# Kernel tuning notes

Measured on AMD Instinct MI355X. Metric: run time of the kernel, lower is better.

The kernel has to match this reference:

```python
import jax, jax.numpy as jnp
import numpy as np
from jax import lax

B, C_IN, H, W = 32, 96, 48, 48
D = C_IN          # d_inner = expand(1) * in_features
K, N, DT_RANK = 2, 16, 6   # k_group, d_state, ceil(D/16)


def setup_inputs() -> dict:
    key = jax.random.key(0)
    ks = jax.random.split(key, 10)
    s = 0.02
    return {
        "x": jax.random.normal(ks[0], (B, C_IN, H, W), jnp.float32),
        "in_proj_w": jax.random.normal(ks[1], (D, C_IN)) * s,
        "in_proj_b": jnp.zeros((D,)),
        "skip_w": jax.random.normal(ks[2], (1, 1, 5)) * s,
        "skip_b": jnp.zeros((1,)),
        "conv2d_w": jax.random.normal(ks[3], (D, 1, 3, 3)) * s,
        "conv2d_b": jnp.zeros((D,)),
        "local_w": jax.random.normal(ks[4], (D, 1, 3, 3)) * s,
        "local_b": jnp.zeros((D,)),
        "bn_gamma": jnp.ones((D,)),
        "bn_beta": jnp.zeros((D,)),
        "x_proj_w": jax.random.normal(ks[5], (K, DT_RANK + 2 * N, D)) * s,
        "dt_projs_w": jax.random.normal(ks[6], (K, D, DT_RANK)) * s,
        "dt_projs_b": jax.random.normal(ks[7], (K, D)) * s,
        "A_logs": jnp.tile(jnp.log(jnp.arange(1, N + 1, dtype=jnp.float32))[None], (K * D, 1)),
        "Ds": jnp.ones((K * D,)),
        "norm_gamma": jnp.ones((D,)),
        "norm_beta": jnp.zeros((D,)),
        "out_proj_w": jax.random.normal(ks[8], (C_IN, D)) * s,
        "out_proj_b": jnp.zeros((C_IN,)),
    }


def _dwconv2d(x, w, bias):
    # depthwise 3x3, NCHW
    y = lax.conv_general_dilated(x, w, (1, 1), "SAME", feature_group_count=x.shape[1],
                                 dimension_numbers=("NCHW", "OIHW", "NCHW"))
    return y + bias[None, :, None, None]


def _forward(x, in_proj_w, in_proj_b, skip_w, skip_b, conv2d_w, conv2d_b,
             local_w, local_b, bn_gamma, bn_beta, x_proj_w, dt_projs_w,
             dt_projs_b, A_logs, Ds, norm_gamma, norm_beta, out_proj_w, out_proj_b):
    b, c, h, w = x.shape
    L = h * w
    x_in = jnp.transpose(x, (0, 2, 3, 1))                       # [B,H,W,C]
    # skip gate: Conv1d(1,1,k=5) over channel axis of the spatial mean
    zm = jnp.mean(x_in, axis=(1, 2))[:, None, :]                # [B,1,C]
    z = lax.conv_general_dilated(zm, skip_w, (1,), "SAME",
                                 dimension_numbers=("NCH", "OIH", "NCH")) + skip_b[None, :, None]
    z = z[:, None]                                              # [B,1,1,C]
    x_feat = jnp.transpose(x_in @ in_proj_w.T + in_proj_b, (0, 3, 1, 2))  # [B,D,H,W]
    x_conv = jax.nn.silu(_dwconv2d(x_feat, conv2d_w, conv2d_b))
    # ---- dynamic center-similarity ordering (computed under no_grad) ----
    xc = lax.stop_gradient(x_conv)
    xf = xc.reshape(b, D, L)
    xn = xf / jnp.maximum(jnp.linalg.norm(xf, axis=1, keepdims=True), 1e-12)
    cf = xc[:, :, h // 2, w // 2]                               # [B,D]
    cn = cf / jnp.maximum(jnp.linalg.norm(cf, axis=1, keepdims=True), 1e-12)
    sim = jnp.einsum("bdl,bd->bl", xn, cn)
    sort_idx = jnp.argsort(-sim, axis=1)                        # descending similarity
    inv_idx = jnp.argsort(sort_idx, axis=1)
    # ---- DynamicCenterScan: sorted sequence and its reverse (k_group=2) ----
    xseq = jnp.take_along_axis(x_conv.reshape(b, D, L), sort_idx[:, None, :], axis=2)
    xs = jnp.stack([xseq, jnp.flip(xseq, -1)], axis=1)          # [B,K,D,L]
    # ---- SS2D selective-scan core ----
    x_dbl = jnp.einsum("bkdl,kcd->bkcl", xs, x_proj_w)
    dts, Bs, Cs = jnp.split(x_dbl, [DT_RANK, DT_RANK + N], axis=2)
    dts = jnp.einsum("bkrl,kdr->bkdl", dts, dt_projs_w)
    dts = jax.nn.softplus(dts + dt_projs_b[None, :, :, None])   # [B,K,D,L]
    A = -jnp.exp(A_logs.reshape(K, D, N))                       # [K,D,N]

    def step(hst, t):
        dt_l, B_l, C_l, x_l = t                                 # [B,K,D],[B,K,N],[B,K,N],[B,K,D]
        dA = jnp.exp(dt_l[..., None] * A)                       # [B,K,D,N]
        hst = dA * hst + (dt_l * x_l)[..., None] * B_l[:, :, None, :]
        y = jnp.einsum("bkdn,bkn->bkd", hst, C_l)
        return hst, y

    tmove = lambda a: jnp.moveaxis(a, -1, 0)
    h0 = jnp.zeros((b, K, D, N), x.dtype)
    _, ys_t = lax.scan(step, h0, (tmove(dts), tmove(Bs), tmove(Cs), tmove(xs)))
    ys = jnp.moveaxis(ys_t, 0, -1) + Ds.reshape(K, D)[None, :, :, None] * xs  # [B,K,D,L]
    # ---- DynamicCenterMerge: un-flip, sum directions, inverse permutation ----
    y = ys[:, 0] + jnp.flip(ys[:, 1], -1)
    y = jnp.take_along_axis(y, inv_idx[:, None, :], axis=2).reshape(b, D, h, w)
    # out_norm: LayerNorm over channels
    yl = jnp.transpose(y, (0, 2, 3, 1))
    mu = jnp.mean(yl, -1, keepdims=True)
    var = jnp.var(yl, -1, keepdims=True)
    yl = (yl - mu) / jnp.sqrt(var + 1e-5) * norm_gamma + norm_beta
    out_mamba = jnp.transpose(yl, (0, 3, 1, 2))
    # local path: depthwise conv + BatchNorm (batch stats, train mode) + SiLU
    lc = _dwconv2d(x_conv, local_w, local_b)
    bm = jnp.mean(lc, (0, 2, 3))
    bv = jnp.var(lc, (0, 2, 3))
    lc = (lc - bm[None, :, None, None]) * (bn_gamma / jnp.sqrt(bv + 1e-5))[None, :, None, None] + bn_beta[None, :, None, None]
    lc = jax.nn.silu(lc)
    out = out_mamba + lc
    # softmax over dim=1 of z (singleton) == all-ones gate; kept for faithfulness
    out = jnp.transpose(out, (0, 2, 3, 1)) * jax.nn.softmax(z, axis=1)
    out = out @ out_proj_w.T + out_proj_b
    return jnp.transpose(out, (0, 3, 1, 2))


def reference(x, in_proj_w, in_proj_b, skip_w, skip_b, conv2d_w, conv2d_b,
              local_w, local_b, bn_gamma, bn_beta, x_proj_w, dt_projs_w,
              dt_projs_b, A_logs, Ds, norm_gamma, norm_beta, out_proj_w, out_proj_b):
    return _forward(x, in_proj_w, in_proj_b, skip_w, skip_b, conv2d_w, conv2d_b,
                    local_w, local_b, bn_gamma, bn_beta, x_proj_w, dt_projs_w,
                    dt_projs_b, A_logs, Ds, norm_gamma, norm_beta, out_proj_w, out_proj_b)
```

## Files before the change

### kernel.cpp

```cpp
#include <hip/hip_runtime.h>
#include <hip/hip_bf16.h>


typedef __hip_bfloat16 bf16;
typedef float v2f __attribute__((ext_vector_type(2)));
typedef float v4f __attribute__((ext_vector_type(4)));
#define SH2(V, a, b) __builtin_shufflevector(V, V, a, b)

__device__ __forceinline__ float b2f(bf16 v) { return __bfloat162float(v); }
__device__ __forceinline__ float ldu(const void* p, int i, bool f32) {
  if (f32) return ((const float*)p)[i];
  return b2f(((const bf16*)p)[i]);
}
__device__ __forceinline__ float rcp_f(float x) { return __builtin_amdgcn_rcpf(x); }

#define LL 2304
#define NSEG 72

#define W_INT  0
#define B_IN   9216
#define W_C2D  9312
#define B_C2D  10176
#define W_LOC  10272
#define B_LOC  11136
#define BN_G   11232
#define BN_B   11328
#define W_XPT  11424
#define W_DT   19104
#define B_DT   20256
#define A2OF   20448
#define DSOF   23520
#define LN_G   23712
#define LN_B   23808
#define W_OUTT 23904
#define B_OUT  33120
#define WBUF_N 33280ul

#define O_WBUF  0ul
#define O_XFEAT 33280ul
#define O_XCONV 7111168ul
#define O_SIM   14189056ul
#define O_SIDX  14262784ul
#define O_XST   14336512ul
#define O_XSTD  21414400ul
#define O_RBUF  28492288ul
#define O_BC    29671936ul
#define O_DSUM  34390528ul
#define O_YMLM  34832896ul
#define O_STATS 41910784ul
#define O_AFLG  41910976ul
#define O_SCSH  41911040ul
#define O_FLAG  41911232ul
#define O_END   41911296ul

__global__ void k_detect(const void* x, float* flag) {
  int i = threadIdx.x;
  bool bad = false;
  const bf16* xb = (const bf16*)x;
#pragma unroll
  for (int r = 0; r < 4; ++r) {
    float v = b2f(xb[r * 64 + i]);
    if (!(fabsf(v) <= 1e4f)) bad = true;
  }
  bool any = __any(bad);
  if (i == 0) flag[0] = any ? 1.f : 0.f;
}

__global__ void k_prep(const void* ipw, const void* ipb, const void* c2w, const void* c2b,
                       const void* lw, const void* lb, const void* bng, const void* bnb,
                       const void* xpw, const void* dtw, const void* dtb, const void* alog,
                       const void* dss, const void* ng, const void* nb, const void* opw,
                       const void* opb, float* wb, const float* flag, float* aflag) {
  bool f = flag[0] > 0.5f;
  int i = blockIdx.x * 256 + threadIdx.x;
  if (i < 9216) {
    int r = i / 96, c = i % 96;
    wb[W_INT + c * 96 + r] = ldu(ipw, i, f);
    wb[W_OUTT + c * 96 + r] = ldu(opw, i, f);
  }
  if (i < 96) {
    wb[B_IN + i] = ldu(ipb, i, f); wb[B_C2D + i] = ldu(c2b, i, f); wb[B_LOC + i] = ldu(lb, i, f);
    wb[BN_G + i] = ldu(bng, i, f); wb[BN_B + i] = ldu(bnb, i, f); wb[LN_G + i] = ldu(ng, i, f);
    wb[LN_B + i] = ldu(nb, i, f); wb[B_OUT + i] = ldu(opb, i, f);
  }
  if (i < 864) { wb[W_C2D + i] = ldu(c2w, i, f); wb[W_LOC + i] = ldu(lw, i, f); }
  if (i < 7296) {
    int k = i / 3648, c = (i / 96) % 38, d = i % 96;
    wb[W_XPT + d * 80 + k * 38 + c] = ldu(xpw, i, f);
  }
  if (i < 1152) wb[W_DT + i] = ldu(dtw, i, f);
  if (i < 192) { wb[B_DT + i] = ldu(dtb, i, f); wb[DSOF + i] = ldu(dss, i, f); }
  if (i < 3072) {
    float av = expf(ldu(alog, i, f));
    wb[A2OF + i] = -av * 1.4426950408889634f;
    int n = i % 16;
    if (fabsf(av - (float)(n + 1)) > 1e-3f * (n + 1)) atomicAdd(aflag, 1.f);
  }
}

__global__ __launch_bounds__(128, 4)
void k_inproj(const void* __restrict__ x, const float* __restrict__ wb,
              float* __restrict__ xfeat, const float* __restrict__ flag) {
  int b = blockIdx.x / 72;
  int rest = blockIdx.x % 72;
  int q = rest / 18;
  int l = (rest % 18) * 128 + threadIdx.x;
  float acc[24];
#pragma unroll
  for (int j = 0; j < 24; ++j) acc[j] = wb[B_IN + q * 24 + j];
  bool f = flag[0] > 0.5f;
  if (f) {
    const float* xf = (const float*)x;
#pragma unroll 2
    for (int c = 0; c < 96; ++c) {
      float xc = xf[(b * 96 + c) * LL + l];
      const float* wr = wb + W_INT + c * 96 + q * 24;
#pragma unroll
      for (int j = 0; j < 24; ++j) acc[j] += xc * wr[j];
    }
  } else {
    const bf16* xb = (const bf16*)x;
#pragma unroll 2
    for (int c = 0; c < 96; ++c) {
      float xc = b2f(xb[(b * 96 + c) * LL + l]);
      const float* wr = wb + W_INT + c * 96 + q * 24;
#pragma unroll
      for (int j = 0; j < 24; ++j) acc[j] += xc * wr[j];
    }
  }
#pragma unroll
  for (int j = 0; j < 24; ++j) xfeat[(b * 96 + q * 24 + j) * LL + l] = acc[j];
}

__global__ __launch_bounds__(256, 8)
void k_conv_silu(const float* __restrict__ xfeat, const float* __restrict__ wb,
                 float* __restrict__ xconv) {
  int t = blockIdx.x * 256 + threadIdx.x;
  int l = t % LL; int d = (t / LL) % 96; int b = t / (LL * 96);
  int h = l / 48, w = l % 48;
  const float* wr = wb + W_C2D + d * 9;
  const float* src = xfeat + (b * 96 + d) * LL;
  float acc = wb[B_C2D + d];
#pragma unroll
  for (int ki = 0; ki < 3; ++ki) {
    int hh = h + ki - 1; if (hh < 0 || hh >= 48) continue;
#pragma unroll
    for (int kj = 0; kj < 3; ++kj) {
      int ww = w + kj - 1; if (ww < 0 || ww >= 48) continue;
      acc += src[hh * 48 + ww] * wr[ki * 3 + kj];
    }
  }
  xconv[t] = acc / (1.f + expf(-acc));
}

__global__ __launch_bounds__(256, 8)
void k_sim(const float* __restrict__ xconv, float* __restrict__ sim) {
  int b = blockIdx.x / 9;
  int l = (blockIdx.x % 9) * 256 + threadIdx.x;
  const float* base = xconv + (size_t)b * 96 * LL;
  float dot = 0, nrm = 0, cn = 0;
  for (int d = 0; d < 96; ++d) {
    float v = base[d * LL + l];
    float c = base[d * LL + 1176];
    dot += v * c; nrm += v * v; cn += c * c;
  }
  float den = fmaxf(sqrtf(nrm), 1e-12f) * fmaxf(sqrtf(cn), 1e-12f);
  sim[b * LL + l] = dot / den;
}

__global__ __launch_bounds__(256, 8)
void k_rank(const float* __restrict__ sim, int* __restrict__ sidx) {
  __shared__ unsigned su[LL];
  int b = blockIdx.x / 36;
  int part = blockIdx.x % 36;
  const float* sp = sim + b * LL;
  for (int i = threadIdx.x; i < LL; i += 256) {
    unsigned u = __float_as_uint(sp[i]);
    u = (u >> 31) ? ~u : (u | 0x80000000u);
    su[i] = u;
  }
  __syncthreads();
  int lq = threadIdx.x >> 2;
  int ch = threadIdx.x & 3;
  int l = part * 64 + lq;
  unsigned ui = su[l];
  int rank = 0;
  const uint4* s4 = (const uint4*)su;
#pragma unroll 4
  for (int it = 0; it < 144; ++it) {
    int m = 4 * it + ch;
    uint4 U = s4[m];
    int j = 4 * m;
    rank += (int)(U.x > ui) + (int)((U.x == ui) & (j + 0 < l));
    rank += (int)(U.y > ui) + (int)((U.y == ui) & (j + 1 < l));
    rank += (int)(U.z > ui) + (int)((U.z == ui) & (j + 2 < l));
    rank += (int)(U.w > ui) + (int)((U.w == ui) & (j + 3 < l));
  }
  rank += __shfl_xor(rank, 1);
  rank += __shfl_xor(rank, 2);
  if (ch == 0) sidx[b * LL + rank] = l;
}

__global__ __launch_bounds__(256, 8)
void k_gatherd(const float* __restrict__ xconv, const int* __restrict__ sidx,
               float* __restrict__ xstd) {
  int t = blockIdx.x * 256 + threadIdx.x;
  int l = t % LL; int d = (t / LL) % 96; int b = t / (LL * 96);
  int p = sidx[b * LL + l];
  xstd[t] = xconv[((size_t)b * 96 + d) * LL + p];
}

__global__ __launch_bounds__(256, 4)
void k_tr_dl(const float* __restrict__ in, float* __restrict__ out) {
  __shared__ float tile[64 * 97];
  int b = blockIdx.x / 36;
  int l0 = (blockIdx.x % 36) * 64;
#pragma unroll
  for (int it = 0; it < 24; ++it) {
    int idx = it * 256 + threadIdx.x;
    int d = idx / 64, j = idx % 64;
    tile[j * 97 + d] = in[((size_t)b * 96 + d) * LL + l0 + j];
  }
  __syncthreads();
#pragma unroll
  for (int it = 0; it < 24; ++it) {
    int idx = it * 256 + threadIdx.x;
    int r = idx / 96, c = idx % 96;
    out[((size_t)b * LL + l0 + r) * 96 + c] = tile[r * 97 + c];
  }
}

__global__ __launch_bounds__(256, 4)
void k_tr_ld(const float* __restrict__ in, float* __restrict__ out) {
  __shared__ float tile[64 * 97];
  int b = blockIdx.x / 36;
  int l0 = (blockIdx.x % 36) * 64;
#pragma unroll
  for (int it = 0; it < 24; ++it) {
    int idx = it * 256 + threadIdx.x;
    int r = idx / 96, c = idx % 96;
    tile[r * 97 + c] = in[((size_t)b * LL + l0 + r) * 96 + c];
  }
  __syncthreads();
#pragma unroll
  for (int it = 0; it < 24; ++it) {
    int idx = it * 256 + threadIdx.x;
    int d = idx / 64, j = idx % 64;
    out[((size_t)b * 96 + d) * LL + l0 + j] = tile[j * 97 + d];
  }
}

__global__ __launch_bounds__(128, 4)
void k_xdbl(const float* __restrict__ xstd, const float* __restrict__ wb,
            float* __restrict__ rbuf, float* __restrict__ bc) {
  int kq = blockIdx.x / 576;
  int r = blockIdx.x % 576;
  int b = r / 18;
  int l = (r % 18) * 128 + threadIdx.x;
  float acc[38];
#pragma unroll
  for (int j = 0; j < 38; ++j) acc[j] = 0.f;
#pragma unroll 2
  for (int c = 0; c < 96; ++c) {
    float xc = xstd[((size_t)b * 96 + c) * LL + l];
    const float* wr = wb + W_XPT + c * 80 + kq * 38;
#pragma unroll
    for (int j = 0; j < 38; ++j) acc[j] += xc * wr[j];
  }
  int lout = kq ? (LL - 1 - l) : l;
  float4* r4 = (float4*)(rbuf + ((size_t)(b * 2 + kq) * LL + lout) * 8);
  r4[0] = make_float4(acc[0], acc[1], acc[2], acc[3]);
  r4[1] = make_float4(acc[4], acc[5], 0.f, 0.f);
  float4* b4 = (float4*)(bc + ((size_t)(b * 2 + kq) * LL + lout) * 32);
#pragma unroll
  for (int i = 0; i < 8; ++i)
    b4[i] = make_float4(acc[6 + 4 * i], acc[7 + 4 * i], acc[8 + 4 * i], acc[9 + 4 * i]);
}

__global__ __launch_bounds__(192, 3)
void k_scan1(const float* __restrict__ rbuf, const float* __restrict__ bc,
             const float* __restrict__ xst, const float* __restrict__ wb,
             float* __restrict__ dsum, float* __restrict__ hend,
             const float* __restrict__ aflag) {
  __shared__ float sbc[2][1024];
  __shared__ float srr[2][256];
  int sub = threadIdx.x / 96;
  int tid = threadIdx.x - sub * 96;
  int unit = blockIdx.x * 2 + sub;
  int s = unit % 72; int k = (unit / 72) % 2; int b = unit / 144;
  int lbase = (b * 2 + k) * LL + s * 32;
  long long lk0 = k ? (LL - 1 - s * 32) : (s * 32);
  long long stp = k ? -96 : 96;
  const float* xp = xst + (size_t)b * LL * 96 + lk0 * 96 + tid;
  float xv[32];
#pragma unroll
  for (int t = 0; t < 32; ++t) xv[t] = xp[t * stp];
  {
    const float4* bsrc = (const float4*)(bc + (size_t)lbase * 32);
    float4* bdst = (float4*)sbc[sub];
    for (int i = tid; i < 256; i += 96) bdst[i] = bsrc[i];
    const float4* rsrc = (const float4*)(rbuf + (size_t)lbase * 8);
    float4* rdst = (float4*)srr[sub];
    if (tid < 64) rdst[tid] = rsrc[tid];
  }
  __syncthreads();
  int d = tid;
  float wd[6];
#pragma unroll
  for (int j = 0; j < 6; ++j) wd[j] = wb[W_DT + (k * 96 + d) * 6 + j];
  float bd = wb[B_DT + k * 96 + d];
  float ds = 0.f;
  v2f h2[8];
#pragma unroll
  for (int j = 0; j < 8; ++j) h2[j] = (v2f){0.f, 0.f};
  bool fast = (aflag[0] == 0.f);
  if (fast) {
    const v4f* bq4 = (const v4f*)sbc[sub];
    const v4f* rq4 = (const v4f*)srr[sub];
#pragma unroll
    for (int t = 0; t < 32; ++t) {
      v4f r0 = rq4[t * 2], r1 = rq4[t * 2 + 1];
      float a = bd + r0.x * wd[0] + r0.y * wd[1] + r0.z * wd[2]
                   + r0.w * wd[3] + r1.x * wd[4] + r1.y * wd[5];
      float ea = __expf(a);
      float p1 = rcp_f(1.f + ea);
      float dtv = (a > 20.f) ? a : -0.69314718055994531f * __log2f(p1);
      ds += dtv;
      float dtx = dtv * xv[t];
      v2f dt2 = {dtx, dtx};
      float p2s = p1 * p1;
      v2f P1 = {p1, p2s};
      v2f P2 = P1 * (v2f){p2s, p2s};
      float p4s = P2.y;
      v2f P3 = P1 * (v2f){p4s, p4s};
      v2f P4 = P2 * (v2f){p4s, p4s};
      float p8s = P4.y;
      v2f P5 = P1 * (v2f){p8s, p8s};
      v2f P6 = P2 * (v2f){p8s, p8s};
      v2f P7 = P3 * (v2f){p8s, p8s};
      v2f P8 = P4 * (v2f){p8s, p8s};
      v4f B0 = bq4[t * 8 + 0], B1 = bq4[t * 8 + 1];
      v4f B2 = bq4[t * 8 + 2], B3 = bq4[t * 8 + 3];
      h2[0] = P1 * h2[0] + dt2 * SH2(B0, 0, 1);
      h2[1] = P2 * h2[1] + dt2 * SH2(B0, 2, 3);
      h2[2] = P3 * h2[2] + dt2 * SH2(B1, 0, 1);
      h2[3] = P4 * h2[3] + dt2 * SH2(B1, 2, 3);
      h2[4] = P5 * h2[4] + dt2 * SH2(B2, 0, 1);
      h2[5] = P6 * h2[5] + dt2 * SH2(B2, 2, 3);
      h2[6] = P7 * h2[6] + dt2 * SH2(B3, 0, 1);
      h2[7] = P8 * h2[7] + dt2 * SH2(B3, 2, 3);
    }
  } else {
    float a2[16], hh[16];
#pragma unroll
    for (int n = 0; n < 16; ++n) { a2[n] = wb[A2OF + (k * 96 + d) * 16 + n]; hh[n] = 0.f; }
#pragma unroll 4
    for (int t = 0; t < 32; ++t) {
      const float* rr = &srr[sub][t * 8];
      float a = bd + rr[0] * wd[0] + rr[1] * wd[1] + rr[2] * wd[2]
                   + rr[3] * wd[3] + rr[4] * wd[4] + rr[5] * wd[5];
      float dtv = (a > 20.f) ? a : log1pf(expf(a));
      ds += dtv;
      float dtx = dtv * xv[t];
      const float* bcl = &sbc[sub][t * 32];
#pragma unroll
      for (int n = 0; n < 16; ++n) hh[n] = exp2f(dtv * a2[n]) * hh[n] + dtx * bcl[n];
    }
#pragma unroll
    for (int j = 0; j < 8; ++j) h2[j] = (v2f){hh[2 * j], hh[2 * j + 1]};
  }
  dsum[((b * 2 + k) * 96 + d) * NSEG + s] = ds;
  float4* ho = (float4*)(hend + (((size_t)(b * 2 + k) * NSEG + s) * 96 + d) * 16);
  ho[0] = make_float4(h2[0].x, h2[0].y, h2[1].x, h2[1].y);
  ho[1] = make_float4(h2[2].x, h2[2].y, h2[3].x, h2[3].y);
  ho[2] = make_float4(h2[4].x, h2[4].y, h2[5].x, h2[5].y);
  ho[3] = make_float4(h2[6].x, h2[6].y, h2[7].x, h2[7].y);
}

__global__ __launch_bounds__(256, 4)
void k_scan2(const float* __restrict__ dsum, const float* __restrict__ hend,
             const float* __restrict__ wb, float* __restrict__ hstart) {
  int t = blockIdx.x * 256 + threadIdx.x;
  int n = t % 16; int d = (t / 16) % 96; int k = (t / 1536) % 2; int b = t / 3072;
  float a2 = wb[A2OF + (k * 96 + d) * 16 + n];
  float h = 0.f;
  int rowd = ((b * 2 + k) * 96 + d) * NSEG;
#pragma unroll 8
  for (int s = 0; s < NSEG; ++s) {
    size_t idx = (((size_t)(b * 2 + k) * NSEG + s) * 96 + d) * 16 + n;
    hstart[idx] = h;
    h = exp2f(a2 * dsum[rowd + s]) * h + hend[idx];
  }
}

__global__ __launch_bounds__(192, 3)
void k_scan3ln(const float* __restrict__ rbuf, const float* __restrict__ bc,
               const float* __restrict__ xst, const float* __restrict__ wb,
               const float* __restrict__ hstart, const int* __restrict__ sidx,
               float* __restrict__ ymlm, const float* __restrict__ aflag) {
  __shared__ float yA[32 * 97];
  __shared__ float yB[32 * 97];
  __shared__ float sbc[2][1024];
  __shared__ float srr[2][256];
  __shared__ float smu[32], srs[32];
  int b = blockIdx.x / NSEG;
  int u = blockIdx.x % NSEG;
  int t = threadIdx.x;
  int sub = t / 96;
  int d = t - sub * 96;
  int k = sub;
  int seg = sub ? (NSEG - 1 - u) : u;
  int lbase = (b * 2 + k) * LL + seg * 32;
  long long lk0 = k ? (LL - 1 - seg * 32) : (seg * 32);
  long long stp = k ? -96 : 96;
  const float* xp = xst + (size_t)b * LL * 96 + lk0 * 96 + d;
  float xv[32];
#pragma unroll
  for (int i = 0; i < 32; ++i) xv[i] = xp[i * stp];
  {
    const float4* bsrc = (const float4*)(bc + (size_t)lbase * 32);
    float4* bdst = (float4*)sbc[sub];
    for (int i = d; i < 256; i += 96) bdst[i] = bsrc[i];
    const float4* rsrc = (const float4*)(rbuf + (size_t)lbase * 8);
    float4* rdst = (float4*)srr[sub];
    if (d < 64) rdst[d] = rsrc[d];
  }
  __syncthreads();
  {
    float* yacc = sub ? yB : yA;
    float wd[6];
#pragma unroll
    for (int j = 0; j < 6; ++j) wd[j] = wb[W_DT + (k * 96 + d) * 6 + j];
    float bd = wb[B_DT + k * 96 + d];
    float Dv = wb[DSOF + k * 96 + d];
    const float* hi = hstart + (((size_t)(b * 2 + k) * NSEG + seg) * 96 + d) * 16;
    bool fast = (aflag[0] == 0.f);
    if (fast) {
      const v4f* hi4 = (const v4f*)hi;
      v4f H0 = hi4[0], H1 = hi4[1], H2 = hi4[2], H3 = hi4[3];
      v2f h2[8];
      h2[0] = SH2(H0, 0, 1); h2[1] = SH2(H0, 2, 3);
      h2[2] = SH2(H1, 0, 1); h2[3] = SH2(H1, 2, 3);
      h2[4] = SH2(H2, 0, 1); h2[5] = SH2(H2, 2, 3);
      h2[6] = SH2(H3, 0, 1); h2[7] = SH2(H3, 2, 3);
      const v4f* bq4 = (const v4f*)sbc[sub];
      const v4f* rq4 = (const v4f*)srr[sub];
#pragma unroll
      for (int i = 0; i < 32; ++i) {
        v4f r0 = rq4[i * 2], r1 = rq4[i * 2 + 1];
        float a = bd + r0.x * wd[0] + r0.y * wd[1] + r0.z * wd[2]
                     + r0.w * wd[3] + r1.x * wd[4] + r1.y * wd[5];
        float ea = __expf(a);
        float p1 = rcp_f(1.f + ea);
        float dtv = (a > 20.f) ? a : -0.69314718055994531f * __log2f(p1);
        float dtx = dtv * xv[i];
        v2f dt2 = {dtx, dtx};
        float p2s = p1 * p1;
        v2f P1 = {p1, p2s};
        v2f P2 = P1 * (v2f){p2s, p2s};
        float p4s = P2.y;
        v2f P3 = P1 * (v2f){p4s, p4s};
        v2f P4 = P2 * (v2f){p4s, p4s};
        float p8s = P4.y;
        v2f P5 = P1 * (v2f){p8s, p8s};
        v2f P6 = P2 * (v2f){p8s, p8s};
        v2f P7 = P3 * (v2f){p8s, p8s};
        v2f P8 = P4 * (v2f){p8s, p8s};
        v4f B0 = bq4[i * 8 + 0], B1 = bq4[i * 8 + 1];
        v4f B2 = bq4[i * 8 + 2], B3 = bq4[i * 8 + 3];
        v4f C0 = bq4[i * 8 + 4], C1 = bq4[i * 8 + 5];
        v4f C2 = bq4[i * 8 + 6], C3 = bq4[i * 8 + 7];
        v2f y2;
        h2[0] = P1 * h2[0] + dt2 * SH2(B0, 0, 1); y2  = h2[0] * SH2(C0, 0, 1);
        h2[1] = P2 * h2[1] + dt2 * SH2(B0, 2, 3); y2 += h2[1] * SH2(C0, 2, 3);
        h2[2] = P3 * h2[2] + dt2 * SH2(B1, 0, 1); y2 += h2[2] * SH2(C1, 0, 1);
        h2[3] = P4 * h2[3] + dt2 * SH2(B1, 2, 3); y2 += h2[3] * SH2(C1, 2, 3);
        h2[4] = P5 * h2[4] + dt2 * SH2(B2, 0, 1); y2 += h2[4] * SH2(C2, 0, 1);
        h2[5] = P6 * h2[5] + dt2 * SH2(B2, 2, 3); y2 += h2[5] * SH2(C2, 2, 3);
        h2[6] = P7 * h2[6] + dt2 * SH2(B3, 0, 1); y2 += h2[6] * SH2(C3, 0, 1);
        h2[7] = P8 * h2[7] + dt2 * SH2(B3, 2, 3); y2 += h2[7] * SH2(C3, 2, 3);
        int qloc = k ? (31 - i) : i;
        yacc[qloc * 97 + d] = y2.x + y2.y + Dv * xv[i];
      }
    } else {
      float a2[16], hh[16];
#pragma unroll
      for (int n = 0; n < 16; ++n) { a2[n] = wb[A2OF + (k * 96 + d) * 16 + n]; hh[n] = hi[n]; }
#pragma unroll 4
      for (int i = 0; i < 32; ++i) {
        const float* rr = &srr[sub][i * 8];
        float a = bd + rr[0] * wd[0] + rr[1] * wd[1] + rr[2] * wd[2]
                     + rr[3] * wd[3] + rr[4] * wd[4] + rr[5] * wd[5];
        float dtv = (a > 20.f) ? a : log1pf(expf(a));
        float dtx = dtv * xv[i];
        const float* bcl = &sbc[sub][i * 32];
        float y = 0.f;
#pragma unroll
        for (int n = 0; n < 16; ++n) {
          hh[n] = exp2f(dtv * a2[n]) * hh[n] + dtx * bcl[n];
          y += hh[n] * bcl[16 + n];
        }
        int qloc = k ? (31 - i) : i;
        yacc[qloc * 97 + d] = y + Dv * xv[i];
      }
    }
  }
  __syncthreads();
  if (t < 32) {
    float sum = 0, ss = 0;
#pragma unroll
    for (int dd = 0; dd < 96; ++dd) {
      float v = yA[t * 97 + dd] + yB[t * 97 + dd];
      sum += v; ss += v * v;
    }
    float mu = sum * (1.f / 96.f);
    float var = ss * (1.f / 96.f) - mu * mu;
    smu[t] = mu;
    srs[t] = rsqrtf(var + 1e-5f);
  }
  __syncthreads();
  {
    int r = t / 6, c0 = (t % 6) * 16;
    int q = u * 32 + r;
    int p = sidx[b * LL + q];
    float mu = smu[r], rs = srs[r];
    float tmp[16];
#pragma unroll
    for (int j = 0; j < 16; ++j) {
      int dd = c0 + j;
      tmp[j] = (yA[r * 97 + dd] + yB[r * 97 + dd] - mu) * rs * wb[LN_G + dd] + wb[LN_B + dd];
    }
    float4* o4 = (float4*)(ymlm + ((size_t)b * LL + p) * 96 + c0);
    o4[0] = make_float4(tmp[0], tmp[1], tmp[2], tmp[3]);
    o4[1] = make_float4(tmp[4], tmp[5], tmp[6], tmp[7]);
    o4[2] = make_float4(tmp[8], tmp[9], tmp[10], tmp[11]);
    o4[3] = make_float4(tmp[12], tmp[13], tmp[14], tmp[15]);
  }
}

__global__ __launch_bounds__(256, 8)
void k_convlc_bn(const float* __restrict__ xconv, const float* __restrict__ wb,
                 float* __restrict__ lcbuf, float* __restrict__ stats) {
  int bd = blockIdx.x;
  int b = bd / 96, d = bd % 96;
  const float* src = xconv + (size_t)(b * 96 + d) * LL;
  const float* wr = wb + W_LOC + d * 9;
  float bias = wb[B_LOC + d];
  float s1 = 0, s2 = 0;
  for (int l = threadIdx.x; l < LL; l += 256) {
    int h = l / 48, w = l % 48;
    float acc = bias;
#pragma unroll
    for (int ki = 0; ki < 3; ++ki) {
      int hh = h + ki - 1; if (hh < 0 || hh >= 48) continue;
#pragma unroll
      for (int kj = 0; kj < 3; ++kj) {
        int ww = w + kj - 1; if (ww < 0 || ww >= 48) continue;
        acc += src[hh * 48 + ww] * wr[ki * 3 + kj];
      }
    }
    lcbuf[(size_t)(b * 96 + d) * LL + l] = acc;
    s1 += acc; s2 += acc * acc;
  }
  __shared__ float r1[256], r2[256];
  r1[threadIdx.x] = s1; r2[threadIdx.x] = s2; __syncthreads();
  for (int o = 128; o > 0; o >>= 1) {
    if (threadIdx.x < o) { r1[threadIdx.x] += r1[threadIdx.x + o]; r2[threadIdx.x] += r2[threadIdx.x + o]; }
    __syncthreads();
  }
  if (threadIdx.x == 0) { atomicAdd(&stats[d], r1[0]); atomicAdd(&stats[96 + d], r2[0]); }
}

__global__ void k_bnfin(const float* __restrict__ stats, const float* __restrict__ wb,
                        float* __restrict__ scsh) {
  int d = threadIdx.x; if (d >= 96) return;
  float mean = stats[d] * (1.f / 73728.f);
  float var = stats[96 + d] * (1.f / 73728.f) - mean * mean;
  float sc = wb[BN_G + d] * rsqrtf(var + 1e-5f);
  scsh[d] = sc; scsh[96 + d] = wb[BN_B + d] - mean * sc;
}

__global__ __launch_bounds__(128, 4)
void k_final(const float* __restrict__ lcbuf, const float* __restrict__ ymdm,
             const float* __restrict__ wb, const float* __restrict__ scsh,
             void* __restrict__ out, const float* __restrict__ flag) {
  int b = blockIdx.x / 72;
  int rest = blockIdx.x % 72;
  int q = rest / 18;
  int l = (rest % 18) * 128 + threadIdx.x;
  float acc[24];
#pragma unroll
  for (int j = 0; j < 24; ++j) acc[j] = wb[B_OUT + q * 24 + j];
#pragma unroll 2
  for (int d = 0; d < 96; ++d) {
    float lc = lcbuf[((size_t)b * 96 + d) * LL + l] * scsh[d] + scsh[96 + d];
    float vd = lc * rcp_f(1.f + __expf(-lc)) + ymdm[((size_t)b * 96 + d) * LL + l];
    const float* wr = wb + W_OUTT + d * 96 + q * 24;
#pragma unroll
    for (int j = 0; j < 24; ++j) acc[j] += vd * wr[j];
  }
  bool f = flag[0] > 0.5f;
  if (f) {
    float* of = (float*)out;
#pragma unroll
    for (int j = 0; j < 24; ++j) of[(b * 96 + q * 24 + j) * LL + l] = acc[j];
  } else {
    bf16* ob = (bf16*)out;
#pragma unroll
    for (int j = 0; j < 24; ++j) ob[(b * 96 + q * 24 + j) * LL + l] = __float2bfloat16(acc[j]);
  }
}

extern "C" void kernel_launch(void* const* d_in, const int* in_sizes, int n_in,
                              void* d_out, int out_size, void* d_ws, size_t ws_size,
                              hipStream_t stream) {
  if (ws_size < O_END * sizeof(float)) return;
  float* ws = (float*)d_ws;
  float* wb    = ws + O_WBUF;
  float* xfeat = ws + O_XFEAT;
  float* xconv = ws + O_XCONV;
  float* sim   = ws + O_SIM;
  int*   sidx  = (int*)(ws + O_SIDX);
  float* xst   = ws + O_XST;
  float* xstd  = ws + O_XSTD;
  float* rbuf  = ws + O_RBUF;
  float* bc    = ws + O_BC;
  float* dsum  = ws + O_DSUM;
  float* ymlm  = ws + O_YMLM;
  float* stats = ws + O_STATS;
  float* aflag = ws + O_AFLG;
  float* scsh  = ws + O_SCSH;
  float* flag  = ws + O_FLAG;
  float* hend   = xfeat;
  float* hstart = xstd;
  float* ymdm   = xfeat;
  float* lcbuf  = xst;

  hipMemsetAsync(stats, 0, 256 * sizeof(float), stream);
  k_detect<<<1, 64, 0, stream>>>(d_in[0], flag);
  k_prep<<<36, 256, 0, stream>>>(
      d_in[1], d_in[2], d_in[5], d_in[6], d_in[7], d_in[8], d_in[9], d_in[10],
      d_in[11], d_in[12], d_in[13], d_in[14], d_in[15], d_in[16], d_in[17], d_in[18],
      d_in[19], wb, flag, aflag);
  k_inproj<<<2304, 128, 0, stream>>>(d_in[0], wb, xfeat, flag);
  k_conv_silu<<<27648, 256, 0, stream>>>(xfeat, wb, xconv);
  k_sim<<<288, 256, 0, stream>>>(xconv, sim);
  k_rank<<<1152, 256, 0, stream>>>(sim, sidx);
  k_gatherd<<<27648, 256, 0, stream>>>(xconv, sidx, xstd);
  k_tr_dl<<<1152, 256, 0, stream>>>(xstd, xst);
  k_xdbl<<<1152, 128, 0, stream>>>(xstd, wb, rbuf, bc);
  k_scan1<<<2304, 192, 0, stream>>>(rbuf, bc, xst, wb, dsum, hend, aflag);
  k_scan2<<<384, 256, 0, stream>>>(dsum, hend, wb, hstart);
  k_scan3ln<<<2304, 192, 0, stream>>>(rbuf, bc, xst, wb, hstart, sidx, ymlm, aflag);
  k_tr_ld<<<1152, 256, 0, stream>>>(ymlm, ymdm);
  k_convlc_bn<<<3072, 256, 0, stream>>>(xconv, wb, lcbuf, stats);
  k_bnfin<<<1, 96, 0, stream>>>(stats, wb, scsh);
  k_final<<<2304, 128, 0, stream>>>(lcbuf, ymdm, wb, scsh, d_out, flag);
}
```

Baseline: 500.8 us.

## Fuse gather with transpose, drop output transpose, parallelize LayerNorm stats

Merges the per-element gather and the D-to-L transpose into one kernel that gathers a tile into shared memory and writes both layouts. It also removes the final L-to-D transpose by having k_final read the L-major buffer directly, and spreads the LayerNorm row reduction across all 192 threads instead of 32. Together these cut two kernel launches and several full-tensor round trips through global memory. The cost is that k_final now reads 96 floats per thread at a stride of 96 floats across lanes, which is an uncoalesced access pattern.

```diff
diff --git a/kernel.cpp b/kernel.cpp
--- a/kernel.cpp
+++ b/kernel.cpp
@@ -201,52 +201,34 @@
   if (ch == 0) sidx[b * LL + rank] = l;
 }
 
-__global__ __launch_bounds__(256, 8)
-void k_gatherd(const float* __restrict__ xconv, const int* __restrict__ sidx,
-               float* __restrict__ xstd) {
-  int t = blockIdx.x * 256 + threadIdx.x;
-  int l = t % LL; int d = (t / LL) % 96; int b = t / (LL * 96);
-  int p = sidx[b * LL + l];
-  xstd[t] = xconv[((size_t)b * 96 + d) * LL + p];
-}
-
 __global__ __launch_bounds__(256, 4)
-void k_tr_dl(const float* __restrict__ in, float* __restrict__ out) {
+void k_gather2(const float* __restrict__ xconv, const int* __restrict__ sidx,
+               float* __restrict__ xstd, float* __restrict__ xst) {
   __shared__ float tile[64 * 97];
+  __shared__ int sp[64];
   int b = blockIdx.x / 36;
   int l0 = (blockIdx.x % 36) * 64;
+  if (threadIdx.x < 64) sp[threadIdx.x] = sidx[b * LL + l0 + threadIdx.x];
+  __syncthreads();
+  const float* base = xconv + (size_t)b * 96 * LL;
 #pragma unroll
   for (int it = 0; it < 24; ++it) {
     int idx = it * 256 + threadIdx.x;
     int d = idx / 64, j = idx % 64;
-    tile[j * 97 + d] = in[((size_t)b * 96 + d) * LL + l0 + j];
+    tile[j * 97 + d] = base[d * LL + sp[j]];
   }
   __syncthreads();
 #pragma unroll
   for (int it = 0; it < 24; ++it) {
     int idx = it * 256 + threadIdx.x;
     int r = idx / 96, c = idx % 96;
-    out[((size_t)b * LL + l0 + r) * 96 + c] = tile[r * 97 + c];
-  }
-}
-
-__global__ __launch_bounds__(256, 4)
-void k_tr_ld(const float* __restrict__ in, float* __restrict__ out) {
-  __shared__ float tile[64 * 97];
-  int b = blockIdx.x / 36;
-  int l0 = (blockIdx.x % 36) * 64;
-#pragma unroll
-  for (int it = 0; it < 24; ++it) {
-    int idx = it * 256 + threadIdx.x;
-    int r = idx / 96, c = idx % 96;
-    tile[r * 97 + c] = in[((size_t)b * LL + l0 + r) * 96 + c];
-  }
-  __syncthreads();
+    xst[((size_t)b * LL + l0 + r) * 96 + c] = tile[r * 97 + c];
+  }
 #pragma unroll
   for (int it = 0; it < 24; ++it) {
     int idx = it * 256 + threadIdx.x;
     int d = idx / 64, j = idx % 64;
-    out[((size_t)b * 96 + d) * LL + l0 + j] = tile[j * 97 + d];
+    xstd[((size_t)b * 96 + d) * LL + l0 + j] = tile[j * 97 + d];
   }
 }
 
@@ -506,14 +488,26 @@
     }
   }
   __syncthreads();
+  {
+    float* p1 = &srr[0][0];
+    float* p2 = &srr[0][0] + 192;
+    int r = t / 6, c0 = (t % 6) * 16;
+    float s = 0, ss = 0;
+#pragma unroll
+    for (int j = 0; j < 16; ++j) {
+      float v = yA[r * 97 + c0 + j] + yB[r * 97 + c0 + j];
+      s += v; ss += v * v;
+    }
+    p1[t] = s; p2[t] = ss;
+  }
+  __syncthreads();
   if (t < 32) {
-    float sum = 0, ss = 0;
-#pragma unroll
-    for (int dd = 0; dd < 96; ++dd) {
-      float v = yA[t * 97 + dd] + yB[t * 97 + dd];
-      sum += v; ss += v * v;
-    }
-    float mu = sum * (1.f / 96.f);
+    const float* p1 = &srr[0][0];
+    const float* p2 = &srr[0][0] + 192;
+    float s = 0, ss = 0;
+#pragma unroll
+    for (int g = 0; g < 6; ++g) { s += p1[t * 6 + g]; ss += p2[t * 6 + g]; }
+    float mu = s * (1.f / 96.f);
     float var = ss * (1.f / 96.f) - mu * mu;
     smu[t] = mu;
     srs[t] = rsqrtf(var + 1e-5f);
@@ -581,20 +575,21 @@
 }
 
 __global__ __launch_bounds__(128, 4)
-void k_final(const float* __restrict__ lcbuf, const float* __restrict__ ymdm,
+void k_final(const float* __restrict__ lcbuf, const float* __restrict__ ymlm,
              const float* __restrict__ wb, const float* __restrict__ scsh,
              void* __restrict__ out, const float* __restrict__ flag) {
   int b = blockIdx.x / 72;
   int rest = blockIdx.x % 72;
   int q = rest / 18;
   int l = (rest % 18) * 128 + threadIdx.x;
+  const float* yrow = ymlm + ((size_t)b * LL + l) * 96;
   float acc[24];
 #pragma unroll
   for (int j = 0; j < 24; ++j) acc[j] = wb[B_OUT + q * 24 + j];
 #pragma unroll 2
   for (int d = 0; d < 96; ++d) {
     float lc = lcbuf[((size_t)b * 96 + d) * LL + l] * scsh[d] + scsh[96 + d];
-    float vd = lc * rcp_f(1.f + __expf(-lc)) + ymdm[((size_t)b * 96 + d) * LL + l];
+    float vd = lc * rcp_f(1.f + __expf(-lc)) + yrow[d];
     const float* wr = wb + W_OUTT + d * 96 + q * 24;
 #pragma unroll
     for (int j = 0; j < 24; ++j) acc[j] += vd * wr[j];
@@ -633,7 +628,6 @@
   float* flag  = ws + O_FLAG;
   float* hend   = xfeat;
   float* hstart = xstd;
-  float* ymdm   = xfeat;
   float* lcbuf  = xst;
 
   hipMemsetAsync(stats, 0, 256 * sizeof(float), stream);
@@ -646,14 +640,12 @@
   k_conv_silu<<<27648, 256, 0, stream>>>(xfeat, wb, xconv);
   k_sim<<<288, 256, 0, stream>>>(xconv, sim);
   k_rank<<<1152, 256, 0, stream>>>(sim, sidx);
-  k_gatherd<<<27648, 256, 0, stream>>>(xconv, sidx, xstd);
-  k_tr_dl<<<1152, 256, 0, stream>>>(xstd, xst);
+  k_gather2<<<1152, 256, 0, stream>>>(xconv, sidx, xstd, xst);
   k_xdbl<<<1152, 128, 0, stream>>>(xstd, wb, rbuf, bc);
   k_scan1<<<2304, 192, 0, stream>>>(rbuf, bc, xst, wb, dsum, hend, aflag);
   k_scan2<<<384, 256, 0, stream>>>(dsum, hend, wb, hstart);
   k_scan3ln<<<2304, 192, 0, stream>>>(rbuf, bc, xst, wb, hstart, sidx, ymlm, aflag);
-  k_tr_ld<<<1152, 256, 0, stream>>>(ymlm, ymdm);
   k_convlc_bn<<<3072, 256, 0, stream>>>(xconv, wb, lcbuf, stats);
   k_bnfin<<<1, 96, 0, stream>>>(stats, wb, scsh);
-  k_final<<<2304, 128, 0, stream>>>(lcbuf, ymdm, wb, scsh, d_out, flag);
-}
+  k_final<<<2304, 128, 0, stream>>>(lcbuf, ymlm, wb, scsh, d_out, flag);
+}
```

After: 613.4 us. 1.22x slower.
